# Kernel tuning notes

Hardware: AMD Instinct MI355X
Metric: run time of the kernel (lower is better)

The kernel has to match this reference:

```python
import jax, jax.numpy as jnp
import numpy as np


def setup_inputs() -> dict:
    key = jax.random.key(0)
    k1, k2 = jax.random.split(key)
    N, D = 131072, 256      # number of feature vectors, feature_dim
    L, K = 4, 1024          # num_levels, num_clusters
    features = jax.random.normal(k1, (N, D), dtype=jnp.float32)
    codebooks = jax.random.normal(k2, (L, K, D), dtype=jnp.float32)
    return {"features": features, "codebooks": codebooks}


def reference(features, codebooks):
    """Residual VQ: per level, assign each vector to its nearest codebook
    center (L2), gather the center, subtract from the residual, accumulate.

    features:  [N, D]
    codebooks: [L, K, D]
    returns quantized reconstruction [N, D] (sum of selected centers).
    """

    def step(carry, cb):
        res, acc = carry
        # argmin over squared L2 distance; drop the constant ||res||^2 term:
        # ||res - c||^2 = ||res||^2 - 2 res.c + ||c||^2
        scores = jnp.sum(cb * cb, axis=1) - 2.0 * jnp.einsum(
            "nd,kd->nk", res, cb
        )  # [N, K]
        idx = jnp.argmin(scores, axis=1)  # [N]
        q = cb[idx]                        # [N, D] gather
        return (res - q, acc + q), None

    init = (features, jnp.zeros_like(features))
    (res, quantized), _ = jax.lax.scan(step, init, codebooks)
    return quantized
```

## Files before the change

### kernel.cpp

```cpp
#include <hip/hip_runtime.h>
#include <hip/hip_bf16.h>
#include <float.h>
#include <limits.h>

#define NROWS 131072
#define DIM   256
#define NLVL  4
#define KC    1024
#define AMB   6.0f
#define GUARD 0.25f
#define REC   18

typedef __attribute__((ext_vector_type(8))) short bf16x8;
typedef __attribute__((ext_vector_type(4))) float f32x4;
typedef __attribute__((ext_vector_type(4))) unsigned short us4;

__device__ __forceinline__ unsigned short f2b(float f){
  __hip_bfloat16 h = __float2bfloat16(f);
  return *reinterpret_cast<unsigned short*>(&h);
}

__device__ __forceinline__ float sqb(float x){
  float s = x * x;
  asm volatile("" : "+v"(s));
  return s;
}

__device__ __forceinline__ bool sless(float a, int ia, float b, int ib){
  return a < b || (a == b && ia < ib);
}

__device__ __forceinline__ void ins4(float (&s)[4], int (&ix)[4], float v, int ci){
  if (v < s[3]){
    s[3]=v; ix[3]=ci;
#pragma unroll
    for (int j = 3; j >= 1; --j){
      if (s[j] < s[j-1]){
        float t=s[j-1]; s[j-1]=s[j]; s[j]=t;
        int u=ix[j-1]; ix[j-1]=ix[j]; ix[j]=u;
      }
    }
  }
}

__global__ void zero8(int* __restrict__ p){
  if (threadIdx.x < 8) p[threadIdx.x] = 0;
}

__global__ void prep_cbb(const float* __restrict__ cb, unsigned short* __restrict__ cbb){
  const int wave = threadIdx.x >> 6, lane = threadIdx.x & 63;
  const int c = blockIdx.x * 4 + wave;
  const size_t off = (size_t)c * DIM + lane * 4;
  const float4 v = *reinterpret_cast<const float4*>(cb + off);
  us4 u = { f2b(v.x), f2b(v.y), f2b(v.z), f2b(v.w) };
  *reinterpret_cast<us4*>(cbb + off) = u;
}

__global__ void prep_cn(const float* __restrict__ cb, float* __restrict__ cnx){
  const int c = blockIdx.x * 64 + threadIdx.x;
  const float* p = cb + (size_t)c * DIM;
  float blk[2];
  for (int b = 0; b < 2; ++b){
    float r[8];
#pragma unroll
    for (int j = 0; j < 8; ++j) r[j] = sqb(p[b*128 + j]);
    for (int i = 8; i < 128; i += 8)
#pragma unroll
      for (int j = 0; j < 8; ++j) r[j] += sqb(p[b*128 + i + j]);
    blk[b] = ((r[0]+r[1]) + (r[2]+r[3])) + ((r[4]+r[5]) + (r[6]+r[7]));
  }
  cnx[c] = blk[0] + blk[1];
}

template<int LVL>
__global__ __launch_bounds__(512, 4)
void rvq_score(const float* __restrict__ feat,
               const float* __restrict__ cb32,
               const unsigned short* __restrict__ cbb_l,
               const float* __restrict__ cnx_l,
               int* __restrict__ idxw,
               int* __restrict__ cnt8,
               int* __restrict__ arecs,
               int* __restrict__ hrows)
{
  __shared__ __align__(16) char smem[65536];
  unsigned short* Bs = (unsigned short*)smem;
  unsigned short* As = (unsigned short*)(smem + 32768);
  float* rowm  = (float*)(smem + 32768);
  int*   cnt_l = (int*)(smem + 32768 + 1024);
  int*   ovf_l = (int*)(smem + 32768 + 1280);
  int*   cand_l= (int*)(smem + 32768 + 1536);
  __shared__ int acnt_s, hcnt_s, abase_s, hbase_s;

  const int tid  = threadIdx.x;
  const int lane = tid & 63;
  const int wave = tid >> 6;
  const int r16  = lane & 15, quad = lane >> 4;
  const int wr   = wave >> 2, wc = wave & 3;
  const int rowbase = (int)blockIdx.x * 64;

  if (tid == 0){ acnt_s = 0; hcnt_s = 0; }

  bf16x8 s0, s1;
  {
#pragma unroll
    for (int it = 0; it < 2; ++it){
      const int i = it*512 + tid, r = i >> 2, c = i & 3;
      const bf16x8 v = *reinterpret_cast<const bf16x8*>(
          cbb_l + (size_t)r * DIM + ((c ^ (r & 3)) << 3));
      if (it == 0) s0 = v; else s1 = v;
    }
  }

  {
    const int row = tid >> 3;
    const int d0 = (tid & 7) * 32;
    const int grow = rowbase + row;
    int hist[NLVL > 1 ? NLVL : 1];
#pragma unroll
    for (int j = 0; j < LVL; ++j) hist[j] = idxw[j * NROWS + grow];
#pragma unroll
    for (int c4 = 0; c4 < 4; ++c4){
      const int d = d0 + c4*8;
      const float* p = feat + (size_t)grow * DIM + d;
      float4 f0 = *reinterpret_cast<const float4*>(p);
      float4 f1 = *reinterpret_cast<const float4*>(p + 4);
#pragma unroll
      for (int j = 0; j < LVL; ++j){
        const float* cp = cb32 + ((size_t)j * KC + hist[j]) * DIM + d;
        const float4 c0 = *reinterpret_cast<const float4*>(cp);
        const float4 c1 = *reinterpret_cast<const float4*>(cp + 4);
        f0.x -= c0.x; f0.y -= c0.y; f0.z -= c0.z; f0.w -= c0.w;
        f1.x -= c1.x; f1.y -= c1.y; f1.z -= c1.z; f1.w -= c1.w;
      }
      bf16x8 b;
      b[0]=(short)f2b(f0.x); b[1]=(short)f2b(f0.y); b[2]=(short)f2b(f0.z); b[3]=(short)f2b(f0.w);
      b[4]=(short)f2b(f1.x); b[5]=(short)f2b(f1.y); b[6]=(short)f2b(f1.z); b[7]=(short)f2b(f1.w);
      *reinterpret_cast<bf16x8*>(&Bs[row*256 + (((d >> 3) ^ (row & 7)) << 3)]) = b;
    }
  }

  f32x4 acc[2][4];
#pragma unroll
  for (int mi = 0; mi < 2; ++mi)
#pragma unroll
    for (int ni = 0; ni < 4; ++ni) acc[mi][ni] = (f32x4){0.f,0.f,0.f,0.f};

  float ts[2][4] = {{FLT_MAX,FLT_MAX,FLT_MAX,FLT_MAX},{FLT_MAX,FLT_MAX,FLT_MAX,FLT_MAX}};
  int   ti[2][4] = {{INT_MAX,INT_MAX,INT_MAX,INT_MAX},{INT_MAX,INT_MAX,INT_MAX,INT_MAX}};

  int buf = 0;
  for (int i = 0; i < 32; ++i){
    const int ct = i >> 3, kt = i & 7;
    __syncthreads();
    {
      const int i0 = tid, r0 = i0 >> 2, c0 = i0 & 3;
      *reinterpret_cast<bf16x8*>(&As[buf*8192 + r0*32 + (c0 << 3)]) = s0;
      const int i1 = 512 + tid, r1 = i1 >> 2, c1 = i1 & 3;
      *reinterpret_cast<bf16x8*>(&As[buf*8192 + r1*32 + (c1 << 3)]) = s1;
    }
    if (i < 31){
      const int ni2 = i + 1, nct = ni2 >> 3, nkt = ni2 & 7;
#pragma unroll
      for (int it = 0; it < 2; ++it){
        const int ii = it*512 + tid, r = ii >> 2, c = ii & 3;
        const bf16x8 v = *reinterpret_cast<const bf16x8*>(
            cbb_l + (size_t)(nct*256 + r) * DIM + nkt*32 + ((c ^ (r & 3)) << 3));
        if (it == 0) s0 = v; else s1 = v;
      }
    }
    __syncthreads();

    bf16x8 Bf[2], Af[4];
#pragma unroll
    for (int mi = 0; mi < 2; ++mi){
      const int row = wr*32 + mi*16 + r16;
      Bf[mi] = *reinterpret_cast<const bf16x8*>(
          &Bs[row*256 + (((kt*4 + quad) ^ (row & 7)) << 3)]);
    }
#pragma unroll
    for (int ni = 0; ni < 4; ++ni){
      const int arow = wc*64 + ni*16 + r16;
      Af[ni] = *reinterpret_cast<const bf16x8*>(
          &As[buf*8192 + arow*32 + ((quad ^ (arow & 3)) << 3)]);
    }
#pragma unroll
    for (int ni = 0; ni < 4; ++ni){
      acc[0][ni] = __builtin_amdgcn_mfma_f32_16x16x32_bf16(Af[ni], Bf[0], acc[0][ni], 0, 0, 0);
      acc[1][ni] = __builtin_amdgcn_mfma_f32_16x16x32_bf16(Af[ni], Bf[1], acc[1][ni], 0, 0, 0);
    }

    if (kt == 7){
#pragma unroll
      for (int mi = 0; mi < 2; ++mi)
#pragma unroll
        for (int ni = 0; ni < 4; ++ni){
          const int c0 = ct*256 + wc*64 + ni*16 + quad*4;
          const float4 cn = *reinterpret_cast<const float4*>(cnx_l + c0);
          const f32x4 a = acc[mi][ni];
          ins4(ts[mi], ti[mi], cn.x - 2.f*a[0], c0+0);
          ins4(ts[mi], ti[mi], cn.y - 2.f*a[1], c0+1);
          ins4(ts[mi], ti[mi], cn.z - 2.f*a[2], c0+2);
          ins4(ts[mi], ti[mi], cn.w - 2.f*a[3], c0+3);
          acc[mi][ni] = (f32x4){0.f,0.f,0.f,0.f};
        }
    }
    buf ^= 1;
  }

  __syncthreads();

#pragma unroll
  for (int mi = 0; mi < 2; ++mi){
    float m = ts[mi][0];
    m = fminf(m, __shfl_xor(m, 16));
    m = fminf(m, __shfl_xor(m, 32));
    if (quad == 0) rowm[(wr*32 + mi*16 + r16)*4 + wc] = m;
  }
  if (tid < 64){ cnt_l[tid] = 0; ovf_l[tid] = 0; }
  __syncthreads();

#pragma unroll
  for (int mi = 0; mi < 2; ++mi){
    const int row = wr*32 + mi*16 + r16;
    const float m1 = fminf(fminf(rowm[row*4], rowm[row*4+1]),
                           fminf(rowm[row*4+2], rowm[row*4+3]));
    const float thr = m1 + AMB;
#pragma unroll
    for (int e = 0; e < 4; ++e){
      if (ts[mi][e] <= thr){
        const int pos = atomicAdd(&cnt_l[row], 1);
        if (pos < 16) cand_l[row*16 + pos] = ti[mi][e];
      }
    }
    if (ts[mi][3] <= thr) ovf_l[row] = 1;
  }
  __syncthreads();

  int apos = -1, hpos = -1, myc = 0;
  if (tid < 64){
    myc = cnt_l[tid];
    if (!ovf_l[tid] && myc == 1){
      idxw[LVL * NROWS + rowbase + tid] = cand_l[tid*16];
    } else if (!ovf_l[tid] && myc <= 16){
      apos = atomicAdd(&acnt_s, 1);
    } else {
      hpos = atomicAdd(&hcnt_s, 1);
    }
  }
  __syncthreads();
  if (tid == 0){
    abase_s = acnt_s ? atomicAdd(&cnt8[LVL], acnt_s) : 0;
    hbase_s = hcnt_s ? atomicAdd(&cnt8[4 + LVL], hcnt_s) : 0;
  }
  __syncthreads();
  if (apos >= 0){
    int* rp = arecs + (size_t)(abase_s + apos) * REC;
    rp[0] = rowbase + tid; rp[1] = myc;
    for (int e = 0; e < myc; ++e) rp[2+e] = cand_l[tid*16 + e];
  }
  if (hpos >= 0) hrows[hbase_s + hpos] = rowbase + tid;
}

template<int LVL>
__global__ __launch_bounds__(256)
void rvq_amb(const float* __restrict__ feat,
             const float* __restrict__ cb32,
             const float* __restrict__ cnx_l,
             int* __restrict__ idxw,
             const int* __restrict__ cnt8,
             const int* __restrict__ arecs)
{
  __shared__ float rres[16][260];
  const int tid = threadIdx.x;
  const int g = tid >> 4, q = tid & 15;
  const int cnt = cnt8[LVL];
  const float* cbl = cb32 + (size_t)LVL * KC * DIM;

  for (int rr = blockIdx.x * 16 + g; rr < cnt; rr += gridDim.x * 16){
    const int* rp = arecs + (size_t)rr * REC;
    const int grow = rp[0];
    const int c = rp[1];

    float4 rv[4];
#pragma unroll
    for (int i4 = 0; i4 < 4; ++i4){
      const int d = q*16 + i4*4;
      float4 w = *reinterpret_cast<const float4*>(feat + (size_t)grow * DIM + d);
#pragma unroll
      for (int j2 = 0; j2 < LVL; ++j2){
        const int kj = idxw[(size_t)j2 * NROWS + grow];
        const float4 cv = *reinterpret_cast<const float4*>(
            cb32 + ((size_t)j2 * KC + kj) * DIM + d);
        w.x -= cv.x; w.y -= cv.y; w.z -= cv.z; w.w -= cv.w;
      }
      rv[i4] = w;
      *reinterpret_cast<float4*>(&rres[g][d]) = w;
    }

    float m1 = FLT_MAX, m2 = FLT_MAX; int i1 = INT_MAX;
    for (int qq = 0; qq < c; ++qq){
      const int ci = rp[2+qq];
      const float* cp = cbl + (size_t)ci * DIM + q*16;
      float pa = 0.f;
#pragma unroll
      for (int j = 0; j < 4; ++j){
        const float4 cv = *reinterpret_cast<const float4*>(cp + j*4);
        pa = fmaf(rv[j].x, cv.x, pa); pa = fmaf(rv[j].y, cv.y, pa);
        pa = fmaf(rv[j].z, cv.z, pa); pa = fmaf(rv[j].w, cv.w, pa);
      }
#pragma unroll
      for (int m = 1; m < 16; m <<= 1) pa += __shfl_xor(pa, m);
      const float sc = cnx_l[ci] - 2.0f * pa;
      if (sless(sc, ci, m1, i1)){ m2 = m1; m1 = sc; i1 = ci; }
      else m2 = fminf(m2, sc);
    }

    int winner = i1;
    if (!(m2 - m1 > GUARD)){
      float bs = FLT_MAX; int bi = INT_MAX;
      for (int k = q; k < c; k += 16){
        const int ci = rp[2+k];
        float a = 0.f;
        for (int d4 = 0; d4 < 64; ++d4){
          const float4 cv = *reinterpret_cast<const float4*>(cbl + (size_t)ci * DIM + d4*4);
          const float4 rw = *reinterpret_cast<const float4*>(&rres[g][d4*4]);
          a = fmaf(rw.x, cv.x, a); a = fmaf(rw.y, cv.y, a);
          a = fmaf(rw.z, cv.z, a); a = fmaf(rw.w, cv.w, a);
        }
        const float sc = cnx_l[ci] - 2.0f * a;
        if (sless(sc, ci, bs, bi)){ bs = sc; bi = ci; }
      }
#pragma unroll
      for (int m = 1; m < 16; m <<= 1){
        const float ob = __shfl_xor(bs, m); const int oi = __shfl_xor(bi, m);
        if (sless(ob, oi, bs, bi)){ bs = ob; bi = oi; }
      }
      winner = bi;
    }
    if (q == 0) idxw[(size_t)LVL * NROWS + grow] = winner;
  }
}

template<int LVL>
__global__ __launch_bounds__(256)
void rvq_hard(const float* __restrict__ feat,
              const float* __restrict__ cb32,
              const float* __restrict__ cnx_l,
              int* __restrict__ idxw,
              const int* __restrict__ cnt8,
              const int* __restrict__ hrows)
{
  __shared__ float rres[260];
  __shared__ float scb[1024];
  __shared__ float wmn[4];
  __shared__ float wbs[4];
  __shared__ int   wbi[4];
  const int tid = threadIdx.x;
  const int g = tid >> 4, q = tid & 15;
  const int wv = tid >> 6, ln = tid & 63;
  const int cnt = cnt8[4 + LVL];
  const float* cbl = cb32 + (size_t)LVL * KC * DIM;

  for (int r = blockIdx.x; r < cnt; r += gridDim.x){
    const int grow = hrows[r];
    if (tid < 16){
#pragma unroll
      for (int i4 = 0; i4 < 4; ++i4){
        const int d = tid*16 + i4*4;
        float4 w = *reinterpret_cast<const float4*>(feat + (size_t)grow * DIM + d);
#pragma unroll
        for (int j2 = 0; j2 < LVL; ++j2){
          const int kj = idxw[(size_t)j2 * NROWS + grow];
          const float4 cv = *reinterpret_cast<const float4*>(
              cb32 + ((size_t)j2 * KC + kj) * DIM + d);
          w.x -= cv.x; w.y -= cv.y; w.z -= cv.z; w.w -= cv.w;
        }
        *reinterpret_cast<float4*>(&rres[d]) = w;
      }
    }
    __syncthreads();

    float4 rv[4];
#pragma unroll
    for (int j = 0; j < 4; ++j)
      rv[j] = *reinterpret_cast<const float4*>(&rres[q*16 + j*4]);

    for (int t = 0; t < 64; ++t){
      const int ci = g*64 + t;
      float pa = 0.f;
#pragma unroll
      for (int j = 0; j < 4; ++j){
        const float4 cv = *reinterpret_cast<const float4*>(
            cbl + (size_t)ci * DIM + q*16 + j*4);
        pa = fmaf(rv[j].x, cv.x, pa); pa = fmaf(rv[j].y, cv.y, pa);
        pa = fmaf(rv[j].z, cv.z, pa); pa = fmaf(rv[j].w, cv.w, pa);
      }
#pragma unroll
      for (int m = 1; m < 16; m <<= 1) pa += __shfl_xor(pa, m);
      if (q == 0) scb[ci] = cnx_l[ci] - 2.0f * pa;
    }
    __syncthreads();

    float mn = fminf(fminf(scb[tid], scb[tid+256]), fminf(scb[tid+512], scb[tid+768]));
#pragma unroll
    for (int m = 1; m < 64; m <<= 1) mn = fminf(mn, __shfl_xor(mn, m));
    if (ln == 0) wmn[wv] = mn;
    __syncthreads();
    const float m1p = fminf(fminf(wmn[0], wmn[1]), fminf(wmn[2], wmn[3]));
    const float thr = m1p + GUARD;

    float bs = FLT_MAX; int bi = INT_MAX;
#pragma unroll
    for (int k = 0; k < 4; ++k){
      const int ci = tid + k*256;
      if (scb[ci] <= thr){
        float a = 0.f;
        for (int d4 = 0; d4 < 64; ++d4){
          const float4 cv = *reinterpret_cast<const float4*>(cbl + (size_t)ci * DIM + d4*4);
          const float4 rw = *reinterpret_cast<const float4*>(&rres[d4*4]);
          a = fmaf(rw.x, cv.x, a); a = fmaf(rw.y, cv.y, a);
          a = fmaf(rw.z, cv.z, a); a = fmaf(rw.w, cv.w, a);
        }
        const float sc = cnx_l[ci] - 2.0f * a;
        if (sless(sc, ci, bs, bi)){ bs = sc; bi = ci; }
      }
    }
#pragma unroll
    for (int m = 1; m < 64; m <<= 1){
      const float ob = __shfl_xor(bs, m); const int oi = __shfl_xor(bi, m);
      if (sless(ob, oi, bs, bi)){ bs = ob; bi = oi; }
    }
    if (ln == 0){ wbs[wv] = bs; wbi[wv] = bi; }
    __syncthreads();
    if (tid == 0){
      float fb = wbs[0]; int fi = wbi[0];
#pragma unroll
      for (int w = 1; w < 4; ++w)
        if (sless(wbs[w], wbi[w], fb, fi)){ fb = wbs[w]; fi = wbi[w]; }
      idxw[(size_t)LVL * NROWS + grow] = fi;
    }
    __syncthreads();
  }
}

__global__ __launch_bounds__(256)
void rvq_out(const float* __restrict__ cb32,
             const int* __restrict__ idxw,
             float* __restrict__ out)
{
  const int tid = threadIdx.x;
  const int row = tid >> 4, sub = tid & 15;
  const size_t n = (size_t)blockIdx.x * 16 + row;
  int hist[NLVL];
#pragma unroll
  for (int j2 = 0; j2 < 4; ++j2) hist[j2] = idxw[(size_t)j2 * NROWS + n];
#pragma unroll
  for (int i = 0; i < 4; ++i){
    const int d = sub*4 + i*64;
    float4 a = *reinterpret_cast<const float4*>(
        cb32 + ((size_t)0 * KC + hist[0]) * DIM + d);
#pragma unroll
    for (int j2 = 1; j2 < 4; ++j2){
      const float4 qv = *reinterpret_cast<const float4*>(
          cb32 + ((size_t)j2 * KC + hist[j2]) * DIM + d);
      a.x += qv.x; a.y += qv.y; a.z += qv.z; a.w += qv.w;
    }
    *reinterpret_cast<float4*>(out + n*DIM + d) = a;
  }
}

extern "C" void kernel_launch(void* const* d_in, const int* in_sizes, int n_in,
                              void* d_out, int out_size, void* d_ws, size_t ws_size,
                              hipStream_t stream){
  const float* feat = (const float*)d_in[0];
  const float* cb32 = (const float*)d_in[1];
  float* out = (float*)d_out;

  char* ws = (char*)d_ws;
  float* cnx  = (float*)(ws);
  int*   cnt8 = (int*)(ws + 16384);
  unsigned short* cbb = (unsigned short*)(ws + 32768);
  int*   idxw = (int*)(ws + 32768 + 2097152);
  int*   arecs = (int*)(ws + 32768 + 2097152 + 2097152);
  int*   hrows = (int*)(ws + 32768 + 2097152 + 2097152 + 9961472);

  zero8<<<1, 64, 0, stream>>>(cnt8);
  prep_cbb<<<1024, 256, 0, stream>>>(cb32, cbb);
  prep_cn<<<64, 64, 0, stream>>>(cb32, cnx);

#define LVL_STEP(L) \
  rvq_score<L><<<2048, 512, 0, stream>>>(feat, cb32, cbb + (size_t)L*KC*DIM, \
      cnx + L*KC, idxw, cnt8, arecs, hrows); \
  rvq_amb<L><<<2048, 256, 0, stream>>>(feat, cb32, cnx + L*KC, idxw, cnt8, arecs); \
  rvq_hard<L><<<512, 256, 0, stream>>>(feat, cb32, cnx + L*KC, idxw, cnt8, hrows);

  LVL_STEP(0)
  LVL_STEP(1)
  LVL_STEP(2)
  LVL_STEP(3)
#undef LVL_STEP

  rvq_out<<<8192, 256, 0, stream>>>(cb32, idxw, out);
}
```

Before: 1.125 ms.

## Stage codebook tiles with direct global-to-LDS loads and drop one barrier

Codebook bf16 tiles were loaded into registers and then written to shared memory. They are now copied straight from global memory into the double-buffered LDS tile with global_load_lds 16-byte transfers, issued for the next tile right after the top-of-loop barrier. This removes the register round trip, the explicit LDS stores and the second __syncthreads per iteration. The XOR swizzle moves to the global-address side, and the per-lane A fragment offsets are precomputed outside the loop. Correctness depends on the barrier waiting for the outstanding async LDS writes before the next tile is consumed.

```diff
diff --git a/kernel.cpp b/kernel.cpp
--- a/kernel.cpp
+++ b/kernel.cpp
@@ -28,6 +28,12 @@
 
 __device__ __forceinline__ bool sless(float a, int ia, float b, int ib){
   return a < b || (a == b && ia < ib);
+}
+
+__device__ __forceinline__ void gld16(const unsigned short* g, unsigned short* l){
+  __builtin_amdgcn_global_load_lds(
+      (const __attribute__((address_space(1))) unsigned int*)g,
+      (__attribute__((address_space(3))) unsigned int*)l, 16, 0, 0);
 }
 
 __device__ __forceinline__ void ins4(float (&s)[4], int (&ix)[4], float v, int ci){
@@ -101,16 +107,22 @@
 
   if (tid == 0){ acnt_s = 0; hcnt_s = 0; }
 
-  bf16x8 s0, s1;
-  {
-#pragma unroll
-    for (int it = 0; it < 2; ++it){
-      const int i = it*512 + tid, r = i >> 2, c = i & 3;
-      const bf16x8 v = *reinterpret_cast<const bf16x8*>(
-          cbb_l + (size_t)r * DIM + ((c ^ (r & 3)) << 3));
-      if (it == 0) s0 = v; else s1 = v;
-    }
-  }
+  const int i0 = tid,        r0 = i0 >> 2, c0i = i0 & 3;
+  const int i1 = 512 + tid,  r1 = i1 >> 2, c1i = i1 & 3;
+  const int x0 = (r0 & 3) ^ ((r0 >> 2) & 3);
+  const int x1 = (r1 & 3) ^ ((r1 >> 2) & 3);
+  const size_t gbase0 = (size_t)r0 * DIM + ((c0i ^ x0) << 3);
+  const size_t gbase1 = (size_t)r1 * DIM + ((c1i ^ x1) << 3);
+  unsigned short* ldst0 = As + i0 * 8;
+  unsigned short* ldst1 = As + i1 * 8;
+
+#define STAGE(TI, B) { \
+    const size_t toff = (size_t)((TI) >> 3) * (256*DIM) + ((TI) & 7) * 32; \
+    gld16(cbb_l + gbase0 + toff, ldst0 + (B)*8192); \
+    gld16(cbb_l + gbase1 + toff, ldst1 + (B)*8192); \
+  }
+
+  STAGE(0, 0)
 
   {
     const int row = tid >> 3;
@@ -149,27 +161,19 @@
   float ts[2][4] = {{FLT_MAX,FLT_MAX,FLT_MAX,FLT_MAX},{FLT_MAX,FLT_MAX,FLT_MAX,FLT_MAX}};
   int   ti[2][4] = {{INT_MAX,INT_MAX,INT_MAX,INT_MAX},{INT_MAX,INT_MAX,INT_MAX,INT_MAX}};
 
+  int offA[4];
+#pragma unroll
+  for (int ni = 0; ni < 4; ++ni){
+    const int arow = wc*64 + ni*16 + r16;
+    const int xa = (arow & 3) ^ ((arow >> 2) & 3);
+    offA[ni] = arow*32 + ((quad ^ xa) << 3);
+  }
+
   int buf = 0;
   for (int i = 0; i < 32; ++i){
     const int ct = i >> 3, kt = i & 7;
     __syncthreads();
-    {
-      const int i0 = tid, r0 = i0 >> 2, c0 = i0 & 3;
-      *reinterpret_cast<bf16x8*>(&As[buf*8192 + r0*32 + (c0 << 3)]) = s0;
-      const int i1 = 512 + tid, r1 = i1 >> 2, c1 = i1 & 3;
-      *reinterpret_cast<bf16x8*>(&As[buf*8192 + r1*32 + (c1 << 3)]) = s1;
-    }
-    if (i < 31){
-      const int ni2 = i + 1, nct = ni2 >> 3, nkt = ni2 & 7;
-#pragma unroll
-      for (int it = 0; it < 2; ++it){
-        const int ii = it*512 + tid, r = ii >> 2, c = ii & 3;
-        const bf16x8 v = *reinterpret_cast<const bf16x8*>(
-            cbb_l + (size_t)(nct*256 + r) * DIM + nkt*32 + ((c ^ (r & 3)) << 3));
-        if (it == 0) s0 = v; else s1 = v;
-      }
-    }
-    __syncthreads();
+    if (i < 31) STAGE(i + 1, buf ^ 1)
 
     bf16x8 Bf[2], Af[4];
 #pragma unroll
@@ -179,11 +183,8 @@
           &Bs[row*256 + (((kt*4 + quad) ^ (row & 7)) << 3)]);
     }
 #pragma unroll
-    for (int ni = 0; ni < 4; ++ni){
-      const int arow = wc*64 + ni*16 + r16;
-      Af[ni] = *reinterpret_cast<const bf16x8*>(
-          &As[buf*8192 + arow*32 + ((quad ^ (arow & 3)) << 3)]);
-    }
+    for (int ni = 0; ni < 4; ++ni)
+      Af[ni] = *reinterpret_cast<const bf16x8*>(&As[buf*8192 + offA[ni]]);
 #pragma unroll
     for (int ni = 0; ni < 4; ++ni){
       acc[0][ni] = __builtin_amdgcn_mfma_f32_16x16x32_bf16(Af[ni], Bf[0], acc[0][ni], 0, 0, 0);
@@ -207,6 +208,7 @@
     }
     buf ^= 1;
   }
+#undef STAGE
 
   __syncthreads();
 
```

Result: slower. 1.149 ms (+2.1%).
